# Kernel optimization log

Hardware: AMD Instinct MI355X
Metric: run time of the kernel (lower is better)

## Reference

```python
import jax, jax.numpy as jnp
import numpy as np
import math

D_MODEL = 1024
NUM_HEADS = 16
HEAD_DIM = D_MODEL // NUM_HEADS
BATCH = 2
SEQ = 2048
NEG_INF = -1000000.0  # matches torch code's -1e6 fill


def setup_inputs() -> dict:
    key = jax.random.key(0)
    ks = jax.random.split(key, 10)
    s = 1.0 / math.sqrt(D_MODEL)
    inp = {
        "X": jax.random.normal(ks[0], (BATCH, SEQ, D_MODEL), dtype=jnp.float32),
        "Wq": jax.random.uniform(ks[1], (D_MODEL, D_MODEL), minval=-s, maxval=s, dtype=jnp.float32),
        "bq": jnp.zeros((D_MODEL,), jnp.float32),
        "Wk": jax.random.uniform(ks[2], (D_MODEL, D_MODEL), minval=-s, maxval=s, dtype=jnp.float32),
        "bk": jnp.zeros((D_MODEL,), jnp.float32),
        "Wv": jax.random.uniform(ks[3], (D_MODEL, D_MODEL), minval=-s, maxval=s, dtype=jnp.float32),
        "bv": jnp.zeros((D_MODEL,), jnp.float32),
        "Wo": jax.random.uniform(ks[4], (D_MODEL, D_MODEL), minval=-s, maxval=s, dtype=jnp.float32),
        "bo": jnp.zeros((D_MODEL,), jnp.float32),
        "valid_lens": jax.random.randint(ks[5], (BATCH, NUM_HEADS), 1, SEQ + 1, dtype=jnp.int64)
        if jax.config.jax_enable_x64 else
        jax.random.randint(ks[5], (BATCH, NUM_HEADS), 1, SEQ + 1, dtype=jnp.int32),
    }
    return inp


def _split_heads(Y, B, S):
    # (B, S, D) -> (B*H, S, head_dim), matching transpose_qkv
    return Y.reshape(B, S, NUM_HEADS, HEAD_DIM).transpose(0, 2, 1, 3).reshape(B * NUM_HEADS, S, HEAD_DIM)


def reference(X, Wq, bq, Wk, bk, Wv, bv, Wo, bo, valid_lens):
    B, S, D = X.shape
    q = _split_heads(X @ Wq.T + bq, B, S)
    k = _split_heads(X @ Wk.T + bk, B, S)
    v = _split_heads(X @ Wv.T + bv, B, S)
    scores = jnp.einsum("bqd,bkd->bqk", q, k) / math.sqrt(HEAD_DIM)  # (B*H, S, S)
    # Faithful to torch code: 2-D valid_lens reshaped to (B*H,), mask over
    # the first two dims -> entire query rows j >= valid_len set to -1e6.
    row_mask = jnp.arange(S)[None, :] < valid_lens.reshape(-1)[:, None]  # (B*H, S)
    scores = jnp.where(row_mask[:, :, None], scores, NEG_INF)
    attn = jax.nn.softmax(scores, axis=-1)
    out = jnp.einsum("bqk,bkd->bqd", attn, v)  # (B*H, S, head_dim)
    out = out.reshape(B, NUM_HEADS, S, HEAD_DIM).transpose(0, 2, 1, 3).reshape(B, S, D)
    return out @ Wo.T + bo
```

## Files before the change

### kernel.cpp

```cpp
#include <hip/hip_runtime.h>

#define SQ 2048
#define DM 1024
#define NH 16
#define HD 64

typedef __bf16 bf16x8 __attribute__((ext_vector_type(8)));
typedef float f32x4 __attribute__((ext_vector_type(4)));
typedef unsigned short u16;
typedef unsigned int u32;

__device__ __forceinline__ u16 f2b(float f) {
  union { float f; u32 u; } c; c.f = f;
  return (u16)((c.u + 0x7FFFu + ((c.u >> 16) & 1u)) >> 16);
}

__device__ __forceinline__ void gll16(const void* g, void* l) {
  __builtin_amdgcn_global_load_lds(
      (const __attribute__((address_space(1))) void*)g,
      (__attribute__((address_space(3))) void*)l, 16, 0, 0);
}

__global__ void __launch_bounds__(256) conv_bf16(
    const float* __restrict__ X,
    const float* __restrict__ Wq, const float* __restrict__ Wk,
    const float* __restrict__ Wv, const float* __restrict__ Wo,
    u16* __restrict__ Xb, u16* __restrict__ Wqb, u16* __restrict__ Wkb,
    u16* __restrict__ Wvb, u16* __restrict__ Wob) {
  const size_t e = ((size_t)blockIdx.x * 256 + threadIdx.x) * 8;
  const float* src; u16* dst; size_t rel;
  if (e < 4194304u)      { src = X;  dst = Xb;  rel = e; }
  else if (e < 5242880u) { src = Wq; dst = Wqb; rel = e - 4194304u; }
  else if (e < 6291456u) { src = Wk; dst = Wkb; rel = e - 5242880u; }
  else if (e < 7340032u) { src = Wv; dst = Wvb; rel = e - 6291456u; }
  else                   { src = Wo; dst = Wob; rel = e - 7340032u; }
  float4 a = *(const float4*)(src + rel);
  float4 b = *(const float4*)(src + rel + 4);
  union { u16 h[8]; uint4 v; } o;
  o.h[0] = f2b(a.x); o.h[1] = f2b(a.y); o.h[2] = f2b(a.z); o.h[3] = f2b(a.w);
  o.h[4] = f2b(b.x); o.h[5] = f2b(b.y); o.h[6] = f2b(b.z); o.h[7] = f2b(b.w);
  *(uint4*)(dst + rel) = o.v;
}

__global__ void __launch_bounds__(256) mean_v2(
    const u16* __restrict__ Vt, const int* __restrict__ vlen,
    u16* __restrict__ Ao, int* __restrict__ wl) {
  __shared__ float part[256];
  __shared__ float smv[64];
  const int bh = blockIdx.x, c8 = blockIdx.y;
  const int t = threadIdx.x, d = t >> 2, c = t & 3;
  const u16* row = Vt + ((size_t)bh * HD + d) * SQ + c * 512;
  float s = 0.f;
  for (int i = 0; i < 64; ++i) {
    bf16x8 v = *(const bf16x8*)(row + i * 8);
    s += ((float)v[0] + (float)v[1]) + ((float)v[2] + (float)v[3])
       + ((float)v[4] + (float)v[5]) + ((float)v[6] + (float)v[7]);
  }
  part[t] = s;
  __syncthreads();
  if (c == 0) {
    const float tot = (part[t] + part[t + 1]) + (part[t + 2] + part[t + 3]);
    smv[d] = tot * (1.0f / 2048.0f);
  }
  __syncthreads();

  const int vl = vlen[bh];
  const int ft = (vl + 63) >> 6;
  const int b = bh >> 4, h = bh & 15;
  const int c16 = t & 15, r16 = t >> 4;
  union { u16 h4[4]; uint2 u; } pv;
#pragma unroll
  for (int j = 0; j < 4; ++j) pv.h4[j] = f2b(smv[c16 * 4 + j]);
  for (int ss = ft * 64 + c8 * 16 + r16; ss < SQ; ss += 128)
    *(uint2*)(Ao + ((size_t)(b * SQ + ss)) * DM + h * HD + c16 * 4) = pv.u;

  if (bh == 0 && c8 == 0) {
    __shared__ int nts[32], off[32];
    if (t < 32) {
      int nt = (vlen[t] + 63) >> 6;
      if (nt > 32) nt = 32;
      nts[t] = nt;
    }
    __syncthreads();
    if (t == 0) {
      int acc = 0;
      for (int i = 0; i < 32; ++i) { off[i] = acc; acc += nts[i]; }
      wl[0] = acc;
    }
    __syncthreads();
    if (t < 32) {
      const int o = off[t], nt = nts[t];
      for (int q = 0; q < nt; ++q) wl[1 + o + q] = (t << 5) | q;
    }
  }
}

__global__ void __launch_bounds__(256, 3) qkv_gemm(
    const u16* __restrict__ Xb, const u16* __restrict__ Wqkv,
    const float* __restrict__ bq, const float* __restrict__ bk, const float* __restrict__ bv,
    const int* __restrict__ vlen,
    u16* __restrict__ Qb, u16* __restrict__ Kb, u16* __restrict__ Vt) {
  __shared__ u16 sA[3][4096];
  __shared__ u16 sB[3][4096];
  const int id = blockIdx.x;
  const int swz = (id & 7) * 96 + (id >> 3);
  const int bx = swz % 24, by = swz / 24;
  const int m0 = by * 128, n0 = bx * 128;
  const int mode = n0 >> 10;
  const float* bias = (mode == 0) ? bq : (mode == 1) ? bk : bv;

  if (mode == 0) {
    const int bb = m0 >> 11, s0 = m0 & 2047, h0 = n0 >> 6;
    if (s0 >= vlen[bb * NH + h0] && s0 >= vlen[bb * NH + h0 + 1]) return;
  }

  const int t = threadIdx.x, l = t & 63, w = t >> 6;
  const int wr = w >> 1, wc = w & 1, lg = l >> 4, li = l & 15;

  int srcOff[2];
#pragma unroll
  for (int j = 0; j < 2; ++j) {
    const int g = w * 2 + j;
    const int row = g * 16 + (l >> 2);
    const int colsrc = ((l & 3) * 8) ^ (((row >> 3) & 1) << 4);
    srcOff[j] = row * DM + colsrc;
  }
  const u16* Abase = Xb + (size_t)m0 * DM;
  const u16* Bbase = Wqkv + (size_t)n0 * DM;

  auto stage = [&](int buf, int kt) {
#pragma unroll
    for (int j = 0; j < 2; ++j) {
      gll16(Abase + srcOff[j] + kt * 32, &sA[buf][(w * 2 + j) * 512]);
      gll16(Bbase + srcOff[j] + kt * 32, &sB[buf][(w * 2 + j) * 512]);
    }
  };

  f32x4 acc[4][4];
  f32x4 z4 = {0.f, 0.f, 0.f, 0.f};
#pragma unroll
  for (int i = 0; i < 4; ++i)
#pragma unroll
    for (int j = 0; j < 4; ++j) acc[i][j] = z4;

  stage(0, 0);
  stage(1, 1);
  for (int kt = 0; kt < 32; ++kt) {
    const int bsel = kt % 3;
    if (kt + 2 < 32) stage((kt + 2) % 3, kt + 2);
    if (kt < 30)      asm volatile("s_waitcnt vmcnt(8)" ::: "memory");
    else if (kt == 30) asm volatile("s_waitcnt vmcnt(4)" ::: "memory");
    else               asm volatile("s_waitcnt vmcnt(0)" ::: "memory");
    __builtin_amdgcn_s_barrier();
    asm volatile("" ::: "memory");

    bf16x8 aF[4], bF[4];
#pragma unroll
    for (int mi = 0; mi < 4; ++mi) {
      const int rl = wr * 64 + mi * 16 + li;
      aF[mi] = *(const bf16x8*)(&sA[bsel][rl * 32 + ((lg * 8) ^ (((rl >> 3) & 1) << 4))]);
    }
#pragma unroll
    for (int ni = 0; ni < 4; ++ni) {
      const int rn = wc * 64 + ni * 16 + li;
      bF[ni] = *(const bf16x8*)(&sB[bsel][rn * 32 + ((lg * 8) ^ (((rn >> 3) & 1) << 4))]);
    }
    __builtin_amdgcn_s_setprio(1);
#pragma unroll
    for (int mi = 0; mi < 4; ++mi)
#pragma unroll
      for (int ni = 0; ni < 4; ++ni)
        acc[mi][ni] = __builtin_amdgcn_mfma_f32_16x16x32_bf16(aF[mi], bF[ni], acc[mi][ni], 0, 0, 0);
    __builtin_amdgcn_s_setprio(0);
    asm volatile("" ::: "memory");
    __builtin_amdgcn_s_barrier();
    asm volatile("" ::: "memory");
  }

#pragma unroll
  for (int mi = 0; mi < 4; ++mi) {
    const int m = m0 + wr * 64 + mi * 16 + lg * 4;
    const int b = m >> 11;
    const int s = m & 2047;
#pragma unroll
    for (int ni = 0; ni < 4; ++ni) {
      const int n = n0 + wc * 64 + ni * 16 + li;
      const int nn = n - (mode << 10);
      const int h = nn >> 6, dd = nn & 63;
      const float bia = bias[nn];
      const size_t bh = (size_t)(b * NH + h);
      if (mode == 2) {
        union { u16 h4[4]; uint2 u; } pk;
#pragma unroll
        for (int r = 0; r < 4; ++r) pk.h4[r] = f2b(acc[mi][ni][r] + bia);
        *(uint2*)(Vt + (bh * HD + dd) * SQ + s) = pk.u;
      } else {
#pragma unroll
        for (int r = 0; r < 4; ++r) {
          const float val = acc[mi][ni][r] + bia;
          const int ss = s + r;
          if (mode == 0) Qb[(bh * SQ + ss) * HD + dd] = f2b(val * 0.180336880f);
          else           Kb[(bh * SQ + ss) * HD + dd] = f2b(val);
        }
      }
    }
  }
}

__global__ void __launch_bounds__(256) out_gemm(
    const u16* __restrict__ Ag, const u16* __restrict__ Wob,
    const float* __restrict__ bo, float* __restrict__ out) {
  __shared__ u16 sA[2][2048];
  __shared__ u16 sB[2][4096];
  const int t = threadIdx.x, l = t & 63, w = t >> 6;
  const int wr = w >> 1, wc = w & 1, lg = l >> 4, li = l & 15;
  const int m0 = blockIdx.y * 64, n0 = blockIdx.x * 128;

  auto stage = [&](int buf, int kt) {
    {
      const int s = w * 64 + l;
      const int r = s >> 2, cc = s & 3;
      gll16(Ag + (size_t)(m0 + r) * DM + kt * 32 + cc * 8, &sA[buf][w * 512]);
    }
#pragma unroll
    for (int c = 0; c < 2; ++c) {
      const int g = w * 2 + c;
      const int s = g * 64 + l;
      const int r = s >> 2, cc = s & 3;
      gll16(Wob + (size_t)(n0 + r) * DM + kt * 32 + cc * 8, &sB[buf][g * 512]);
    }
  };

  f32x4 acc[2][4];
  f32x4 z4 = {0.f, 0.f, 0.f, 0.f};
#pragma unroll
  for (int i = 0; i < 2; ++i)
#pragma unroll
    for (int j = 0; j < 4; ++j) acc[i][j] = z4;

  stage(0, 0);
  __syncthreads();
  int cur = 0;
  for (int kt = 0; kt < DM / 32; ++kt) {
    if (kt + 1 < DM / 32) stage(cur ^ 1, kt + 1);
    bf16x8 aF[2], bF[4];
#pragma unroll
    for (int mi = 0; mi < 2; ++mi)
      aF[mi] = *(const bf16x8*)(&sA[cur][(wr * 32 + mi * 16 + li) * 32 + lg * 8]);
#pragma unroll
    for (int ni = 0; ni < 4; ++ni)
      bF[ni] = *(const bf16x8*)(&sB[cur][(wc * 64 + ni * 16 + li) * 32 + lg * 8]);
#pragma unroll
    for (int mi = 0; mi < 2; ++mi)
#pragma unroll
      for (int ni = 0; ni < 4; ++ni)
        acc[mi][ni] = __builtin_amdgcn_mfma_f32_16x16x32_bf16(aF[mi], bF[ni], acc[mi][ni], 0, 0, 0);
    __syncthreads();
    cur ^= 1;
  }

#pragma unroll
  for (int mi = 0; mi < 2; ++mi) {
    const int m = m0 + wr * 32 + mi * 16 + lg * 4;
#pragma unroll
    for (int ni = 0; ni < 4; ++ni) {
      const int n = n0 + wc * 64 + ni * 16 + li;
      const float bia = bo[n];
#pragma unroll
      for (int r = 0; r < 4; ++r)
        out[(size_t)(m + r) * DM + n] = acc[mi][ni][r] + bia;
    }
  }
}

__global__ void __launch_bounds__(256, 2) attn_v15(
    const u16* __restrict__ Qb, const u16* __restrict__ Kb, const u16* __restrict__ Vt,
    const int* __restrict__ vlen, const int* __restrict__ wl, u16* __restrict__ Ao) {
  __shared__ u16 sKV[4][10240];
  const int t = threadIdx.x, w = t >> 6, l = t & 63, lg = l >> 4, li = l & 15;
  const int nit = wl[0];

  int kOff[4], vOff[4];
#pragma unroll
  for (int i = 0; i < 4; ++i) {
    {
      const int s = i * 64 + l, row = s >> 3, c = s & 7;
      const int csrc = c ^ (row & 7);
      const int sig = (((row >> 2) & 3) << 3) | (((row >> 4) & 1) << 2) | (row & 3);
      kOff[i] = sig * HD + csrc * 8;
    }
    {
      const int s = i * 64 + l, d = s >> 2, c = s & 3;
      const int csrc = c ^ ((d >> 2) & 3);
      vOff[i] = d * SQ + csrc * 8;
    }
  }

  u16* sw = &sKV[w][0];
  f32x4* op = (f32x4*)&sKV[0][0];
  float* lp = (float*)((char*)&sKV[0][0] + 65536);

  for (int it = blockIdx.x; it < nit; it += gridDim.x) {
    const int item = wl[1 + it];
    const int bh = item >> 5, qt = item & 31;
    const int vl = vlen[bh];
    const int q0 = qt * 64;
    const int b = bh >> 4, h = bh & 15;
    const u16* Qh = Qb + (size_t)bh * SQ * HD;
    const u16* Kh = Kb + (size_t)bh * SQ * HD;
    const u16* Vh = Vt + (size_t)bh * HD * SQ;
    const int k0 = w * 512;

    bf16x8 qf[4][2];
#pragma unroll
    for (int g = 0; g < 4; ++g) {
      const bool mq = (q0 + g * 16 + li) >= vl;
#pragma unroll
      for (int kk = 0; kk < 2; ++kk) {
        qf[g][kk] = *(const bf16x8*)(Qh + (size_t)(q0 + g * 16 + li) * HD + kk * 32 + lg * 8);
        if (mq) {
          union { u32 u[4]; bf16x8 v; } z; z.u[0] = z.u[1] = z.u[2] = z.u[3] = 0;
          qf[g][kk] = z.v;
        }
      }
    }

    auto stageK = [&](int buf, int tt) {
      const u16* kb = Kh + (size_t)(k0 + tt * 32) * HD;
#pragma unroll
      for (int i = 0; i < 4; ++i) gll16(kb + kOff[i], sw + buf * 2048 + i * 512);
    };
    auto stageV = [&](int buf, int tt) {
      const u16* vb = Vh + (size_t)(k0 + tt * 32);
#pragma unroll
      for (int i = 0; i < 4; ++i) gll16(vb + vOff[i], sw + 6144 + buf * 2048 + i * 512);
    };

    f32x4 z4 = {0.f, 0.f, 0.f, 0.f};
    f32x4 acc[4][4];
    float lr[4] = {0.f, 0.f, 0.f, 0.f};
#pragma unroll
    for (int g = 0; g < 4; ++g)
#pragma unroll
      for (int n2 = 0; n2 < 4; ++n2) acc[g][n2] = z4;

    stageV(0, 0); stageK(0, 0); stageK(1, 1);
    for (int tt = 0; tt < 16; ++tt) {
      if (tt + 1 < 16) stageV((tt + 1) & 1, tt + 1);
      if (tt + 2 < 16) stageK((tt + 2) % 3, tt + 2);
      if (tt <= 13)      asm volatile("s_waitcnt vmcnt(12)" ::: "memory");
      else if (tt == 14) asm volatile("s_waitcnt vmcnt(8)" ::: "memory");
      else               asm volatile("s_waitcnt vmcnt(0)" ::: "memory");
      const u16* kb_ = sw + (tt % 3) * 2048;
      const u16* vb_ = sw + 6144 + (tt & 1) * 2048;

      bf16x8 kf[2][2], vf[4];
#pragma unroll
      for (int ni = 0; ni < 2; ++ni) {
        const int row = ni * 16 + li;
        kf[ni][0] = *(const bf16x8*)(kb_ + row * 64 + ((lg ^ (row & 7)) * 8));
        kf[ni][1] = *(const bf16x8*)(kb_ + row * 64 + (((4 + lg) ^ (row & 7)) * 8));
      }
#pragma unroll
      for (int n2 = 0; n2 < 4; ++n2) {
        const int d = n2 * 16 + li;
        vf[n2] = *(const bf16x8*)(vb_ + d * 32 + ((lg ^ ((d >> 2) & 3)) * 8));
      }

      f32x4 s0a[4], s1a[4];
      __builtin_amdgcn_s_setprio(1);
#pragma unroll
      for (int g = 0; g < 4; ++g) {
        s0a[g] = __builtin_amdgcn_mfma_f32_16x16x32_bf16(kf[0][0], qf[g][0], z4, 0, 0, 0);
        s1a[g] = __builtin_amdgcn_mfma_f32_16x16x32_bf16(kf[1][0], qf[g][0], z4, 0, 0, 0);
      }
#pragma unroll
      for (int g = 0; g < 4; ++g) {
        s0a[g] = __builtin_amdgcn_mfma_f32_16x16x32_bf16(kf[0][1], qf[g][1], s0a[g], 0, 0, 0);
        s1a[g] = __builtin_amdgcn_mfma_f32_16x16x32_bf16(kf[1][1], qf[g][1], s1a[g], 0, 0, 0);
      }
      __builtin_amdgcn_s_setprio(0);

      bf16x8 Pv[4];
#pragma unroll
      for (int g = 0; g < 4; ++g) {
        union { __bf16 e[8]; bf16x8 v; } P;
        float ls = 0.f;
#pragma unroll
        for (int r = 0; r < 4; ++r) {
          const float p0 = __builtin_amdgcn_exp2f(s0a[g][r]);
          const float p1 = __builtin_amdgcn_exp2f(s1a[g][r]);
          P.e[r]     = (__bf16)p0;
          P.e[4 + r] = (__bf16)p1;
          ls += p0 + p1;
        }
        lr[g] += ls;
        Pv[g] = P.v;
      }

      __builtin_amdgcn_s_setprio(1);
#pragma unroll
      for (int g = 0; g < 4; ++g)
#pragma unroll
        for (int n2 = 0; n2 < 4; ++n2)
          acc[g][n2] = __builtin_amdgcn_mfma_f32_16x16x32_bf16(vf[n2], Pv[g], acc[g][n2], 0, 0, 0);
      __builtin_amdgcn_s_setprio(0);
    }

    __syncthreads();
#pragma unroll
    for (int g = 0; g < 4; ++g) {
#pragma unroll
      for (int n2 = 0; n2 < 4; ++n2)
        op[(((w * 4) + g) * 4 + n2) * 64 + l] = acc[g][n2];
      float v = lr[g];
      v += __shfl_xor(v, 16);
      v += __shfl_xor(v, 32);
      if (lg == 0) lp[(w * 4 + g) * 16 + li] = v;
    }
    __syncthreads();

    const int g = w;
    const float lf = lp[(0 * 4 + g) * 16 + li] + lp[(1 * 4 + g) * 16 + li]
                   + lp[(2 * 4 + g) * 16 + li] + lp[(3 * 4 + g) * 16 + li];
    const float inv = 1.0f / lf;
    const size_t rowb = ((size_t)(b * SQ + q0 + g * 16 + li)) * DM + h * HD;
#pragma unroll
    for (int n2 = 0; n2 < 4; ++n2) {
      f32x4 s = op[((0 * 4 + g) * 4 + n2) * 64 + l];
      s += op[((1 * 4 + g) * 4 + n2) * 64 + l];
      s += op[((2 * 4 + g) * 4 + n2) * 64 + l];
      s += op[((3 * 4 + g) * 4 + n2) * 64 + l];
      union { __bf16 h2[4]; uint2 u; } ov;
#pragma unroll
      for (int r = 0; r < 4; ++r) ov.h2[r] = (__bf16)(s[r] * inv);
      *(uint2*)(Ao + rowb + n2 * 16 + lg * 4) = ov.u;
    }
    __syncthreads();
  }
}

extern "C" void kernel_launch(void* const* d_in, const int* in_sizes, int n_in,
                              void* d_out, int out_size, void* d_ws, size_t ws_size,
                              hipStream_t stream) {
  const float* X  = (const float*)d_in[0];
  const float* Wq = (const float*)d_in[1];
  const float* bq = (const float*)d_in[2];
  const float* Wk = (const float*)d_in[3];
  const float* bk = (const float*)d_in[4];
  const float* Wv = (const float*)d_in[5];
  const float* bv = (const float*)d_in[6];
  const float* Wo = (const float*)d_in[7];
  const float* bo = (const float*)d_in[8];
  const int* vlen = (const int*)d_in[9];

  char* ws = (char*)d_ws;
  u16* Qb  = (u16*)(ws);
  u16* Kb  = (u16*)(ws + (size_t)8388608);
  u16* Vt  = (u16*)(ws + (size_t)16777216);
  u16* Xb  = (u16*)(ws + (size_t)25165824);
  u16* Ao  = Xb;
  u16* Wqb = (u16*)(ws + (size_t)33554432);
  u16* Wkb = (u16*)(ws + (size_t)35651584);
  u16* Wvb = (u16*)(ws + (size_t)37748736);
  u16* Wob = (u16*)(ws + (size_t)39845888);

  int* wl = (int*)((char*)d_out + 8192);

  dim3 blk(256);
  conv_bf16<<<4096, blk, 0, stream>>>(X, Wq, Wk, Wv, Wo, Xb, Wqb, Wkb, Wvb, Wob);
  qkv_gemm<<<768, blk, 0, stream>>>(Xb, Wqb, bq, bk, bv, vlen, Qb, Kb, Vt);
  mean_v2<<<dim3(32, 8), blk, 0, stream>>>(Vt, vlen, Ao, wl);
  attn_v15<<<512, blk, 0, stream>>>(Qb, Kb, Vt, vlen, wl, Ao);
  out_gemm<<<dim3(8, 64), blk, 0, stream>>>(Ao, Wob, bo, (float*)d_out);
}
```

Measured before the change: 116.5 us.

## Widen QKV GEMM tile to 128x256 with double buffering

Changes the fused QKV projection GEMM from 128x128 tiles with triple-buffered LDS to 128x256 tiles with double buffering, halving the grid to 384 blocks. Each wave now computes a 64x128 sub-tile, which raises MFMA work per LDS A-fragment load and lowers global A traffic. The early-exit check for masked Q tiles now spans four heads. The costs are more accumulator registers under launch_bounds(256,3), fewer blocks to spread across CUs, and a shallower prefetch pipeline that may expose more memory latency.

```diff
diff --git a/kernel.cpp b/kernel.cpp
--- a/kernel.cpp
+++ b/kernel.cpp
@@ -95,81 +95,88 @@
   }
 }
 
-__global__ void __launch_bounds__(256, 3) qkv_gemm(
+__global__ void __launch_bounds__(256, 3) qkv_gemm2(
     const u16* __restrict__ Xb, const u16* __restrict__ Wqkv,
     const float* __restrict__ bq, const float* __restrict__ bk, const float* __restrict__ bv,
     const int* __restrict__ vlen,
     u16* __restrict__ Qb, u16* __restrict__ Kb, u16* __restrict__ Vt) {
-  __shared__ u16 sA[3][4096];
-  __shared__ u16 sB[3][4096];
+  __shared__ u16 sA[2][4096];
+  __shared__ u16 sB[2][8192];
   const int id = blockIdx.x;
-  const int swz = (id & 7) * 96 + (id >> 3);
-  const int bx = swz % 24, by = swz / 24;
-  const int m0 = by * 128, n0 = bx * 128;
+  const int swz = (id & 7) * 48 + (id >> 3);
+  const int bx = swz % 12, by = swz / 12;
+  const int m0 = by * 128, n0 = bx * 256;
   const int mode = n0 >> 10;
   const float* bias = (mode == 0) ? bq : (mode == 1) ? bk : bv;
 
   if (mode == 0) {
-    const int bb = m0 >> 11, s0 = m0 & 2047, h0 = n0 >> 6;
-    if (s0 >= vlen[bb * NH + h0] && s0 >= vlen[bb * NH + h0 + 1]) return;
+    const int bb = m0 >> 11, s0 = m0 & 2047, h0 = (n0 & 1023) >> 6;
+    if (s0 >= vlen[bb * NH + h0]     && s0 >= vlen[bb * NH + h0 + 1] &&
+        s0 >= vlen[bb * NH + h0 + 2] && s0 >= vlen[bb * NH + h0 + 3]) return;
   }
 
   const int t = threadIdx.x, l = t & 63, w = t >> 6;
   const int wr = w >> 1, wc = w & 1, lg = l >> 4, li = l & 15;
 
-  int srcOff[2];
+  int aOff[2], bOff[4];
 #pragma unroll
   for (int j = 0; j < 2; ++j) {
-    const int g = w * 2 + j;
-    const int row = g * 16 + (l >> 2);
+    const int ch = w * 2 + j;
+    const int row = ch * 16 + (l >> 2);
     const int colsrc = ((l & 3) * 8) ^ (((row >> 3) & 1) << 4);
-    srcOff[j] = row * DM + colsrc;
+    aOff[j] = row * DM + colsrc;
+  }
+#pragma unroll
+  for (int j = 0; j < 4; ++j) {
+    const int ch = w * 4 + j;
+    const int row = ch * 16 + (l >> 2);
+    const int colsrc = ((l & 3) * 8) ^ (((row >> 3) & 1) << 4);
+    bOff[j] = row * DM + colsrc;
   }
   const u16* Abase = Xb + (size_t)m0 * DM;
   const u16* Bbase = Wqkv + (size_t)n0 * DM;
 
   auto stage = [&](int buf, int kt) {
 #pragma unroll
-    for (int j = 0; j < 2; ++j) {
-      gll16(Abase + srcOff[j] + kt * 32, &sA[buf][(w * 2 + j) * 512]);
-      gll16(Bbase + srcOff[j] + kt * 32, &sB[buf][(w * 2 + j) * 512]);
-    }
+    for (int j = 0; j < 2; ++j)
+      gll16(Abase + aOff[j] + kt * 32, &sA[buf][(w * 2 + j) * 512]);
+#pragma unroll
+    for (int j = 0; j < 4; ++j)
+      gll16(Bbase + bOff[j] + kt * 32, &sB[buf][(w * 4 + j) * 512]);
   };
 
-  f32x4 acc[4][4];
+  f32x4 acc[4][8];
   f32x4 z4 = {0.f, 0.f, 0.f, 0.f};
 #pragma unroll
   for (int i = 0; i < 4; ++i)
 #pragma unroll
-    for (int j = 0; j < 4; ++j) acc[i][j] = z4;
+    for (int j = 0; j < 8; ++j) acc[i][j] = z4;
 
   stage(0, 0);
-  stage(1, 1);
   for (int kt = 0; kt < 32; ++kt) {
-    const int bsel = kt % 3;
-    if (kt + 2 < 32) stage((kt + 2) % 3, kt + 2);
-    if (kt < 30)      asm volatile("s_waitcnt vmcnt(8)" ::: "memory");
-    else if (kt == 30) asm volatile("s_waitcnt vmcnt(4)" ::: "memory");
-    else               asm volatile("s_waitcnt vmcnt(0)" ::: "memory");
+    if (kt + 1 < 32) stage((kt + 1) & 1, kt + 1);
+    if (kt + 1 < 32) asm volatile("s_waitcnt vmcnt(6)" ::: "memory");
+    else             asm volatile("s_waitcnt vmcnt(0)" ::: "memory");
     __builtin_amdgcn_s_barrier();
     asm volatile("" ::: "memory");
 
-    bf16x8 aF[4], bF[4];
+    const int bsel = kt & 1;
+    bf16x8 aF[4], bF[8];
 #pragma unroll
     for (int mi = 0; mi < 4; ++mi) {
       const int rl = wr * 64 + mi * 16 + li;
       aF[mi] = *(const bf16x8*)(&sA[bsel][rl * 32 + ((lg * 8) ^ (((rl >> 3) & 1) << 4))]);
     }
 #pragma unroll
-    for (int ni = 0; ni < 4; ++ni) {
-      const int rn = wc * 64 + ni * 16 + li;
+    for (int ni = 0; ni < 8; ++ni) {
+      const int rn = wc * 128 + ni * 16 + li;
       bF[ni] = *(const bf16x8*)(&sB[bsel][rn * 32 + ((lg * 8) ^ (((rn >> 3) & 1) << 4))]);
     }
     __builtin_amdgcn_s_setprio(1);
 #pragma unroll
     for (int mi = 0; mi < 4; ++mi)
 #pragma unroll
-      for (int ni = 0; ni < 4; ++ni)
+      for (int ni = 0; ni < 8; ++ni)
         acc[mi][ni] = __builtin_amdgcn_mfma_f32_16x16x32_bf16(aF[mi], bF[ni], acc[mi][ni], 0, 0, 0);
     __builtin_amdgcn_s_setprio(0);
     asm volatile("" ::: "memory");
@@ -183,9 +190,9 @@
     const int b = m >> 11;
     const int s = m & 2047;
 #pragma unroll
-    for (int ni = 0; ni < 4; ++ni) {
-      const int n = n0 + wc * 64 + ni * 16 + li;
-      const int nn = n - (mode << 10);
+    for (int ni = 0; ni < 8; ++ni) {
+      const int n = n0 + wc * 128 + ni * 16 + li;
+      const int nn = n & 1023;
       const int h = nn >> 6, dd = nn & 63;
       const float bia = bias[nn];
       const size_t bh = (size_t)(b * NH + h);
@@ -469,7 +476,7 @@
 
   dim3 blk(256);
   conv_bf16<<<4096, blk, 0, stream>>>(X, Wq, Wk, Wv, Wo, Xb, Wqb, Wkb, Wvb, Wob);
-  qkv_gemm<<<768, blk, 0, stream>>>(Xb, Wqb, bq, bk, bv, vlen, Qb, Kb, Vt);
+  qkv_gemm2<<<384, blk, 0, stream>>>(Xb, Wqb, bq, bk, bv, vlen, Qb, Kb, Vt);
   mean_v2<<<dim3(32, 8), blk, 0, stream>>>(Vt, vlen, Ao, wl);
   attn_v15<<<512, blk, 0, stream>>>(Qb, Kb, Vt, vlen, wl, Ao);
   out_gemm<<<dim3(8, 64), blk, 0, stream>>>(Ao, Wob, bo, (float*)d_out);
```

New measurement: 159.2 us. 36.6% more time.
